# Optimization experiments

Hardware: AMD Instinct MI355X
Metric: run time of the kernel (lower is better)

## Reference

```python
import jax, jax.numpy as jnp
import numpy as np

N_NODES = 200_000
N_BONDS = 200_000
N_EDGES = 2 * N_BONDS
D_V, D_E, D_H, DEPTH = 133, 14, 200, 3


def setup_inputs() -> dict:
    key = jax.random.key(0)
    ks = jax.random.split(key, 10)
    V = jax.random.normal(ks[0], (N_NODES, D_V), dtype=jnp.float32)
    E_feat = jax.random.normal(ks[1], (N_EDGES, D_E), dtype=jnp.float32)
    # paired directed edges: edge 2b = (u,v), edge 2b+1 = (v,u)
    u = jax.random.randint(ks[2], (N_BONDS,), 0, N_NODES)
    v = jax.random.randint(ks[3], (N_BONDS,), 0, N_NODES)
    src = jnp.stack([u, v], axis=1).reshape(-1)
    dst = jnp.stack([v, u], axis=1).reshape(-1)
    edge_index = jnp.stack([src, dst], axis=0).astype(jnp.int64)
    rev_edge_index = (jnp.arange(N_EDGES) ^ 1).astype(jnp.int64)
    s = 0.05
    W_i = jax.random.normal(ks[4], (D_V + D_E, D_H), dtype=jnp.float32) * s
    b_i = jax.random.normal(ks[5], (D_H,), dtype=jnp.float32) * s
    W_h = jax.random.normal(ks[6], (D_H, D_H), dtype=jnp.float32) * s
    b_h = jax.random.normal(ks[7], (D_H,), dtype=jnp.float32) * s
    W_o = jax.random.normal(ks[8], (D_V + D_H, D_H), dtype=jnp.float32) * s
    b_o = jax.random.normal(ks[9], (D_H,), dtype=jnp.float32) * s
    return {"V": V, "E_feat": E_feat, "edge_index": edge_index,
            "rev_edge_index": rev_edge_index, "W_i": W_i, "b_i": b_i,
            "W_h": W_h, "b_h": b_h, "W_o": W_o, "b_o": b_o}


def reference(V, E_feat, edge_index, rev_edge_index, W_i, b_i, W_h, b_h, W_o, b_o):
    src = edge_index[0]
    dst = edge_index[1]
    n_edges = E_feat.shape[0]
    # h^(0) = relu(W_i([x_v || e_vw]))
    H0 = jax.nn.relu(jnp.concatenate([V[src], E_feat], axis=1) @ W_i + b_i)
    H = H0
    not_self_rev = (rev_edge_index != jnp.arange(n_edges))[:, None]  # [E,1]
    for _ in range(1, DEPTH):
        node_messages = jax.ops.segment_sum(H, dst, num_segments=N_NODES)  # [N,d_h]
        M = node_messages[src] - jnp.where(not_self_rev, H[rev_edge_index], 0.0)
        H = jax.nn.relu(H0 + M @ W_h + b_h)
    M_v = jax.ops.segment_sum(H, src, num_segments=N_NODES)  # [N,d_h]
    H_v = jax.nn.relu(jnp.concatenate([V, M_v], axis=1) @ W_o + b_o)
    return H_v
```

## Files before the change

kernel.cpp:

```cpp
#include <hip/hip_runtime.h>
#include <hip/hip_bf16.h>
#include <stdint.h>

typedef __hip_bfloat16 bf16;
typedef __attribute__((ext_vector_type(8))) short short8;
typedef __attribute__((ext_vector_type(4))) float f32x4;

#define NN 200000
#define NE 400000
#define DV 133
#define DE 14
#define DH 200
#define MT 128
#define NT 13
#define LDA 40
#define NCH 782

#define KI 160
#define KH 224
#define KO 352

#define MFMA(a, b, c) __builtin_amdgcn_mfma_f32_16x16x32_bf16((a), (b), (c), 0, 0, 0)

__device__ __forceinline__ float b2f(bf16 x) { return __bfloat162float(x); }
__device__ __forceinline__ float us2f(unsigned short u) {
  return __uint_as_float(((unsigned)u) << 16);
}
__device__ __forceinline__ unsigned short f2us(float f) {
  bf16 h = __float2bfloat16(f);
  return *reinterpret_cast<unsigned short*>(&h);
}

__global__ __launch_bounds__(256) void prepw_kernel(
    const float* __restrict__ W, int K, int ldk, bf16* __restrict__ out)
{
  int idx = blockIdx.x * 256 + threadIdx.x;
  int rowv = ldk >> 3;
  int total = 208 * rowv;
  if (idx >= total) return;
  int c = idx / rowv, r = idx - c * rowv;
  int k0 = r * 8;
  short8 w;
#pragma unroll
  for (int j = 0; j < 8; ++j) {
    int k = k0 + j;
    float v = (k < K && c < DH) ? W[(size_t)k * DH + c] : 0.f;
    w[j] = (short)f2us(v);
  }
  *(short8*)&((unsigned short*)out)[(size_t)c * ldk + k0] = w;
}

__global__ __launch_bounds__(256) void hist_kernel(
    const int* __restrict__ dst, int* __restrict__ counts)
{
  int e = blockIdx.x * 256 + threadIdx.x;
  if (e < NE) atomicAdd(&counts[dst[e]], 1);
}

__global__ __launch_bounds__(256) void chunksum_kernel(
    const int* __restrict__ counts, int* __restrict__ chunkSum)
{
  int b = blockIdx.x, tid = threadIdx.x;
  int i = b * 256 + tid;
  int v = (i < NN) ? counts[i] : 0;
#pragma unroll
  for (int d = 32; d; d >>= 1) v += __shfl_down(v, d, 64);
  __shared__ int ws[4];
  if ((tid & 63) == 0) ws[tid >> 6] = v;
  __syncthreads();
  if (tid == 0) chunkSum[b] = ws[0] + ws[1] + ws[2] + ws[3];
}

__global__ __launch_bounds__(1024) void scanchunks_kernel(
    const int* __restrict__ chunkSum, int* __restrict__ chunkOff)
{
  __shared__ int s[1024];
  int tid = threadIdx.x;
  int v = (tid < NCH) ? chunkSum[tid] : 0;
  s[tid] = v;
  __syncthreads();
  for (int d = 1; d < 1024; d <<= 1) {
    int t = (tid >= d) ? s[tid - d] : 0;
    __syncthreads();
    s[tid] += t;
    __syncthreads();
  }
  if (tid < NCH) chunkOff[tid] = s[tid] - v;
}

__global__ __launch_bounds__(256) void scanlocal_kernel(
    const int* __restrict__ counts, const int* __restrict__ chunkOff,
    int* __restrict__ offsets, int* __restrict__ cursor)
{
  __shared__ int s[256];
  int b = blockIdx.x, tid = threadIdx.x;
  int i = b * 256 + tid;
  int v = (i < NN) ? counts[i] : 0;
  s[tid] = v;
  __syncthreads();
  for (int d = 1; d < 256; d <<= 1) {
    int t = (tid >= d) ? s[tid - d] : 0;
    __syncthreads();
    s[tid] += t;
    __syncthreads();
  }
  if (i < NN) {
    int off = chunkOff[b] + s[tid] - v;
    offsets[i] = off;
    cursor[i] = off;
  }
  if (i == 0) offsets[NN] = NE;
}

__global__ __launch_bounds__(256) void scatter_kernel(
    const int* __restrict__ dst, int* __restrict__ cursor, int* __restrict__ perm)
{
  int e = blockIdx.x * 256 + threadIdx.x;
  if (e < NE) {
    int p = atomicAdd(&cursor[dst[e]], 1);
    perm[p] = e;
  }
}

__global__ __launch_bounds__(256) void h0_kernel(
    const float* __restrict__ V, const float* __restrict__ Ef,
    const int* __restrict__ src,
    const bf16* __restrict__ WiT,
    const float* __restrict__ bi,
    bf16* __restrict__ H0)
{
  __shared__ __align__(16) unsigned short AsS[MT * LDA];
  __shared__ __align__(16) unsigned short WtS[208 * LDA];
  __shared__ int Ssrc[MT];
  __shared__ float Sb[DH];
  const int tid = threadIdx.x;
  const int e0 = blockIdx.x * MT;
  if (tid < MT) Ssrc[tid] = src[e0 + tid];
  if (tid < DH) Sb[tid] = bi[tid];
  const int wv = tid >> 6, ln = tid & 15, q = (tid & 63) >> 4;
  f32x4 acc[NT][2];
#pragma unroll
  for (int t = 0; t < NT; ++t)
#pragma unroll
    for (int m = 0; m < 2; ++m) acc[t][m] = (f32x4){0.f, 0.f, 0.f, 0.f};
  const int K = DV + DE;
  const unsigned short* Wp = (const unsigned short*)WiT;
  __syncthreads();
  for (int k0 = 0; k0 < KI; k0 += 32) {
    for (int idx = tid; idx < 832; idx += 256) {
      int c = idx >> 2, kg = idx & 3;
      *(short8*)&WtS[c * LDA + kg * 8] =
          *(const short8*)&Wp[(size_t)c * KI + k0 + kg * 8];
    }
    {
      int rr = tid >> 1, half = tid & 1;
      int e = e0 + rr, s = Ssrc[rr];
      int kb = k0 + half * 16;
      unsigned short av[16];
#pragma unroll
      for (int j = 0; j < 16; ++j) {
        int k = kb + j;
        float a = 0.f;
        if (k < DV) a = V[(size_t)s * DV + k];
        else if (k < K) a = Ef[(size_t)e * DE + (k - DV)];
        av[j] = f2us(a);
      }
      short8 w0, w1;
#pragma unroll
      for (int j = 0; j < 8; ++j) { w0[j] = (short)av[j]; w1[j] = (short)av[8 + j]; }
      *(short8*)&AsS[rr * LDA + half * 16] = w0;
      *(short8*)&AsS[rr * LDA + half * 16 + 8] = w1;
    }
    __syncthreads();
    {
      short8 a0 = *(const short8*)&AsS[(wv * 32 + ln) * LDA + q * 8];
      short8 a1 = *(const short8*)&AsS[(wv * 32 + 16 + ln) * LDA + q * 8];
#pragma unroll
      for (int t = 0; t < NT; ++t) {
        short8 b = *(const short8*)&WtS[(t * 16 + ln) * LDA + q * 8];
        acc[t][0] = MFMA(a0, b, acc[t][0]);
        acc[t][1] = MFMA(a1, b, acc[t][1]);
      }
    }
    __syncthreads();
  }
#pragma unroll
  for (int t = 0; t < NT; ++t) {
    int c = t * 16 + ln;
    if (c < DH) {
#pragma unroll
      for (int m = 0; m < 2; ++m)
#pragma unroll
        for (int i = 0; i < 4; ++i) {
          int e = e0 + wv * 32 + m * 16 + q * 4 + i;
          float h = acc[t][m][i] + Sb[c];
          H0[(size_t)e * DH + c] = __float2bfloat16(h > 0.f ? h : 0.f);
        }
    }
  }
}

__global__ __launch_bounds__(256) void gemmq_kernel(
    const bf16* __restrict__ H,
    const bf16* __restrict__ WhT,
    bf16* __restrict__ Q)
{
  __shared__ __align__(16) unsigned short AsS[MT * LDA];
  __shared__ __align__(16) unsigned short WtS[208 * LDA];
  const int tid = threadIdx.x;
  const int e0 = blockIdx.x * MT;
  const int wv = tid >> 6, ln = tid & 15, q = (tid & 63) >> 4;
  f32x4 acc[NT][2];
#pragma unroll
  for (int t = 0; t < NT; ++t)
#pragma unroll
    for (int m = 0; m < 2; ++m) acc[t][m] = (f32x4){0.f, 0.f, 0.f, 0.f};
  const unsigned short* Hs = (const unsigned short*)H;
  const unsigned short* Wp = (const unsigned short*)WhT;
  for (int k0 = 0; k0 < KH; k0 += 32) {
    for (int idx = tid; idx < 832; idx += 256) {
      int c = idx >> 2, kg = idx & 3;
      *(short8*)&WtS[c * LDA + kg * 8] =
          *(const short8*)&Wp[(size_t)c * KH + k0 + kg * 8];
    }
    for (int idx = tid; idx < 512; idx += 256) {
      int rr = idx >> 2, kg = idx & 3;
      *(short8*)&AsS[rr * LDA + kg * 8] =
          *(const short8*)&Hs[(size_t)(e0 + rr) * DH + k0 + kg * 8];
    }
    __syncthreads();
    {
      short8 a0 = *(const short8*)&AsS[(wv * 32 + ln) * LDA + q * 8];
      short8 a1 = *(const short8*)&AsS[(wv * 32 + 16 + ln) * LDA + q * 8];
#pragma unroll
      for (int t = 0; t < NT; ++t) {
        short8 b = *(const short8*)&WtS[(t * 16 + ln) * LDA + q * 8];
        acc[t][0] = MFMA(a0, b, acc[t][0]);
        acc[t][1] = MFMA(a1, b, acc[t][1]);
      }
    }
    __syncthreads();
  }
#pragma unroll
  for (int t = 0; t < NT; ++t) {
    int c = t * 16 + ln;
    if (c < DH) {
#pragma unroll
      for (int m = 0; m < 2; ++m)
#pragma unroll
        for (int i = 0; i < 4; ++i) {
          int e = e0 + wv * 32 + m * 16 + q * 4 + i;
          Q[(size_t)e * DH + c] = __float2bfloat16(acc[t][m][i]);
        }
    }
  }
}

__global__ __launch_bounds__(256) void fusedmp_kernel(
    const bf16* __restrict__ Q, const bf16* H0,
    const int* __restrict__ offsets, const int* __restrict__ perm,
    const float* __restrict__ bh, bf16* Hout)
{
  int t = blockIdx.x * 256 + threadIdx.x;
  if (t >= NN * 25) return;
  int n = t / 25, g = t - n * 25;
  int st = offsets[n], en = offsets[n + 1];
  if (st == en) return;
  const unsigned short* Qs = (const unsigned short*)Q;
  const unsigned short* H0s = (const unsigned short*)H0;
  unsigned short* Os = (unsigned short*)Hout;
  float a[8];
  const float4* bp = (const float4*)(bh + g * 8);
  float4 b0 = bp[0], b1 = bp[1];
  a[0] = b0.x; a[1] = b0.y; a[2] = b0.z; a[3] = b0.w;
  a[4] = b1.x; a[5] = b1.y; a[6] = b1.z; a[7] = b1.w;
  for (int j = st; j < en; ++j) {
    int e = perm[j];
    short8 u = *(const short8*)(Qs + (size_t)e * DH + g * 8);
#pragma unroll
    for (int k = 0; k < 8; ++k) a[k] += us2f((unsigned short)u[k]);
  }
  for (int j = st; j < en; ++j) {
    int e = perm[j];
    int eo = e ^ 1;
    short8 uq = *(const short8*)(Qs + (size_t)e * DH + g * 8);
    short8 uh = *(const short8*)(H0s + (size_t)eo * DH + g * 8);
    short8 w;
#pragma unroll
    for (int k = 0; k < 8; ++k) {
      float h = a[k] - us2f((unsigned short)uq[k]) + us2f((unsigned short)uh[k]);
      w[k] = (short)f2us(h > 0.f ? h : 0.f);
    }
    *(short8*)(Os + (size_t)eo * DH + g * 8) = w;
  }
}

__global__ __launch_bounds__(256) void gather_kernel(
    const bf16* __restrict__ H, const int* __restrict__ offsets,
    const int* __restrict__ perm, int xm, float* __restrict__ nm)
{
  int t = blockIdx.x * 256 + threadIdx.x;
  if (t >= NN * 25) return;
  int n = t / 25, g = t - n * 25;
  int st = offsets[n], en = offsets[n + 1];
  float a[8];
#pragma unroll
  for (int k = 0; k < 8; ++k) a[k] = 0.f;
  const unsigned short* Hs = (const unsigned short*)H;
  for (int j = st; j < en; ++j) {
    int e = perm[j] ^ xm;
    short8 u = *(const short8*)(Hs + (size_t)e * DH + g * 8);
#pragma unroll
    for (int k = 0; k < 8; ++k) a[k] += us2f((unsigned short)u[k]);
  }
  float4* o = (float4*)(nm + (size_t)n * DH + g * 8);
  o[0] = make_float4(a[0], a[1], a[2], a[3]);
  o[1] = make_float4(a[4], a[5], a[6], a[7]);
}

__global__ __launch_bounds__(256) void out_kernel(
    const float* __restrict__ V, const float* __restrict__ Mv,
    const bf16* __restrict__ WoT,
    const float* __restrict__ bo,
    float* __restrict__ out)
{
  __shared__ __align__(16) unsigned short AsS[MT * LDA];
  __shared__ __align__(16) unsigned short WtS[208 * LDA];
  __shared__ float Sb[DH];
  const int tid = threadIdx.x;
  const int n0 = blockIdx.x * MT;
  if (tid < DH) Sb[tid] = bo[tid];
  const int wv = tid >> 6, ln = tid & 15, q = (tid & 63) >> 4;
  f32x4 acc[NT][2];
#pragma unroll
  for (int t = 0; t < NT; ++t)
#pragma unroll
    for (int m = 0; m < 2; ++m) acc[t][m] = (f32x4){0.f, 0.f, 0.f, 0.f};
  const int K = DV + DH;
  const unsigned short* Wp = (const unsigned short*)WoT;
  __syncthreads();
  for (int k0 = 0; k0 < KO; k0 += 32) {
    for (int idx = tid; idx < 832; idx += 256) {
      int c = idx >> 2, kg = idx & 3;
      *(short8*)&WtS[c * LDA + kg * 8] =
          *(const short8*)&Wp[(size_t)c * KO + k0 + kg * 8];
    }
    {
      int rr = tid >> 1, half = tid & 1;
      int n = n0 + rr;
      int kb = k0 + half * 16;
      unsigned short av[16];
      if (n < NN) {
#pragma unroll
        for (int j = 0; j < 16; ++j) {
          int k = kb + j;
          float a = 0.f;
          if (k < DV) a = V[(size_t)n * DV + k];
          else if (k < K) a = Mv[(size_t)n * DH + (k - DV)];
          av[j] = f2us(a);
        }
      } else {
#pragma unroll
        for (int j = 0; j < 16; ++j) av[j] = 0;
      }
      short8 w0, w1;
#pragma unroll
      for (int j = 0; j < 8; ++j) { w0[j] = (short)av[j]; w1[j] = (short)av[8 + j]; }
      *(short8*)&AsS[rr * LDA + half * 16] = w0;
      *(short8*)&AsS[rr * LDA + half * 16 + 8] = w1;
    }
    __syncthreads();
    {
      short8 a0 = *(const short8*)&AsS[(wv * 32 + ln) * LDA + q * 8];
      short8 a1 = *(const short8*)&AsS[(wv * 32 + 16 + ln) * LDA + q * 8];
#pragma unroll
      for (int t = 0; t < NT; ++t) {
        short8 b = *(const short8*)&WtS[(t * 16 + ln) * LDA + q * 8];
        acc[t][0] = MFMA(a0, b, acc[t][0]);
        acc[t][1] = MFMA(a1, b, acc[t][1]);
      }
    }
    __syncthreads();
  }
#pragma unroll
  for (int t = 0; t < NT; ++t) {
    int c = t * 16 + ln;
    if (c < DH) {
#pragma unroll
      for (int m = 0; m < 2; ++m)
#pragma unroll
        for (int i = 0; i < 4; ++i) {
          int n = n0 + wv * 32 + m * 16 + q * 4 + i;
          if (n < NN) {
            float h = acc[t][m][i] + Sb[c];
            out[(size_t)n * DH + c] = h > 0.f ? h : 0.f;
          }
        }
    }
  }
}

extern "C" void kernel_launch(void* const* d_in, const int* in_sizes, int n_in,
                              void* d_out, int out_size, void* d_ws, size_t ws_size,
                              hipStream_t stream)
{
  const float* V  = (const float*)d_in[0];
  const float* Ef = (const float*)d_in[1];
  const int* eidx = (const int*)d_in[2];
  const int* rev  = (const int*)d_in[3];   (void)rev;
  const float* Wi = (const float*)d_in[4];
  const float* bi = (const float*)d_in[5];
  const float* Wh = (const float*)d_in[6];
  const float* bh = (const float*)d_in[7];
  const float* Wo = (const float*)d_in[8];
  const float* bo = (const float*)d_in[9];
  const int* src = eidx;
  const int* dst = eidx + NE;

  bf16* H0 = (bf16*)d_ws;
  bf16* Hb = H0 + (size_t)NE * DH;
  bf16* Q  = Hb + (size_t)NE * DH;
  float* nm = (float*)Q;
  int* counts   = (int*)(Q + (size_t)NE * DH);
  int* chunkSum = counts + NN;
  int* chunkOff = chunkSum + 1024;
  int* offsets  = chunkOff + 1024;
  int* cursor   = offsets + NN + 1;
  int* perm     = cursor + NN;
  bf16* WiT = (bf16*)(((uintptr_t)(perm + NE) + 15) & ~(uintptr_t)15);
  bf16* WhT = WiT + 208 * KI;
  bf16* WoT = WhT + 208 * KH;

  const int gGE = NE / MT;
  const int gON = (NN + MT - 1) / MT;
  const int gE  = (NE + 255) / 256;
  const int gN  = (NN + 255) / 256;
  const int gG  = (NN * 25 + 255) / 256;

  hipMemsetAsync(counts, 0, (size_t)NN * sizeof(int), stream);
  hist_kernel<<<gE, 256, 0, stream>>>(dst, counts);
  chunksum_kernel<<<NCH, 256, 0, stream>>>(counts, chunkSum);
  scanchunks_kernel<<<1, 1024, 0, stream>>>(chunkSum, chunkOff);
  scanlocal_kernel<<<gN, 256, 0, stream>>>(counts, chunkOff, offsets, cursor);
  scatter_kernel<<<gE, 256, 0, stream>>>(dst, cursor, perm);

  prepw_kernel<<<(208 * KI / 8 + 255) / 256, 256, 0, stream>>>(Wi, DV + DE, KI, WiT);
  prepw_kernel<<<(208 * KH / 8 + 255) / 256, 256, 0, stream>>>(Wh, DH, KH, WhT);
  prepw_kernel<<<(208 * KO / 8 + 255) / 256, 256, 0, stream>>>(Wo, DV + DH, KO, WoT);

  h0_kernel<<<gGE, 256, 0, stream>>>(V, Ef, src, WiT, bi, H0);

  gemmq_kernel<<<gGE, 256, 0, stream>>>(H0, WhT, Q);
  fusedmp_kernel<<<gG, 256, 0, stream>>>(Q, H0, offsets, perm, bh, Hb);

  gemmq_kernel<<<gGE, 256, 0, stream>>>(Hb, WhT, Q);
  fusedmp_kernel<<<gG, 256, 0, stream>>>(Q, H0, offsets, perm, bh, H0);

  gather_kernel<<<gG, 256, 0, stream>>>(H0, offsets, perm, 1, nm);
  out_kernel<<<gON, 256, 0, stream>>>(V, nm, WoT, bo, (float*)d_out);
}
```

Measured before the change: 1.392 ms.

## Pre-pack V and output GEMM operand as padded bf16 rows for vectorized loads

Adds a pass that converts V to a bf16 buffer padded to 160 columns. The h0 GEMM gathers source-node rows from it with 16-byte vector loads instead of scalar fp32 loads and per-element conversion. For the output stage, the gather kernel writes M_v as bf16 straight into a combined [M_v || V] padded operand, with Wo rows reordered to match, so out_kernel streams A tiles with vector loads. This costs extra pack kernels, and the workspace buffers are reused, which adds aliasing risk.

```diff
diff --git a/kernel.cpp b/kernel.cpp
--- a/kernel.cpp
+++ b/kernel.cpp
@@ -7,6 +7,7 @@
 typedef __attribute__((ext_vector_type(4))) float f32x4;
 
 #define NN 200000
+#define NNPAD 200064
 #define NE 400000
 #define DV 133
 #define DE 14
@@ -19,10 +20,10 @@
 #define KI 160
 #define KH 224
 #define KO 352
+#define LDV 160
 
 #define MFMA(a, b, c) __builtin_amdgcn_mfma_f32_16x16x32_bf16((a), (b), (c), 0, 0, 0)
 
-__device__ __forceinline__ float b2f(bf16 x) { return __bfloat162float(x); }
 __device__ __forceinline__ float us2f(unsigned short u) {
   return __uint_as_float(((unsigned)u) << 16);
 }
@@ -48,6 +49,60 @@
     w[j] = (short)f2us(v);
   }
   *(short8*)&((unsigned short*)out)[(size_t)c * ldk + k0] = w;
+}
+
+__global__ __launch_bounds__(256) void prepwo_kernel(
+    const float* __restrict__ Wo, bf16* __restrict__ out)
+{
+  int idx = blockIdx.x * 256 + threadIdx.x;
+  int total = 208 * (KO >> 3);
+  if (idx >= total) return;
+  int c = idx / (KO >> 3), r = idx - c * (KO >> 3);
+  int k0 = r * 8;
+  short8 w;
+#pragma unroll
+  for (int j = 0; j < 8; ++j) {
+    int k = k0 + j;
+    int sr = (k < 200) ? (133 + k) : (k - 200);
+    float v = (k < 333 && c < DH) ? Wo[(size_t)sr * DH + c] : 0.f;
+    w[j] = (short)f2us(v);
+  }
+  *(short8*)&((unsigned short*)out)[(size_t)c * KO + k0] = w;
+}
+
+__global__ __launch_bounds__(256) void packv_kernel(
+    const float* __restrict__ V, unsigned short* __restrict__ Vb)
+{
+  int idx = blockIdx.x * 256 + threadIdx.x;
+  if (idx >= NN * (LDV / 8)) return;
+  int n = idx / (LDV / 8), g = idx - n * (LDV / 8);
+  int k0 = g * 8;
+  short8 w;
+#pragma unroll
+  for (int j = 0; j < 8; ++j) {
+    int k = k0 + j;
+    float v = (k < DV) ? V[(size_t)n * DV + k] : 0.f;
+    w[j] = (short)f2us(v);
+  }
+  *(short8*)&Vb[(size_t)n * LDV + k0] = w;
+}
+
+__global__ __launch_bounds__(256) void packav_kernel(
+    const float* __restrict__ V, unsigned short* __restrict__ Abuf)
+{
+  int idx = blockIdx.x * 256 + threadIdx.x;
+  if (idx >= NNPAD * (KO / 8)) return;
+  int n = idx / (KO / 8), g = idx - n * (KO / 8);
+  int k0 = g * 8;
+  if (n < NN && k0 < 200) return;
+  short8 w;
+#pragma unroll
+  for (int j = 0; j < 8; ++j) {
+    int k = k0 + j;
+    float v = (n < NN && k >= 200 && k < 333) ? V[(size_t)n * DV + (k - 200)] : 0.f;
+    w[j] = (short)f2us(v);
+  }
+  *(short8*)&Abuf[(size_t)n * KO + k0] = w;
 }
 
 __global__ __launch_bounds__(256) void hist_kernel(
@@ -123,7 +178,8 @@
 }
 
 __global__ __launch_bounds__(256) void h0_kernel(
-    const float* __restrict__ V, const float* __restrict__ Ef,
+    const unsigned short* __restrict__ Vb,
+    const float* __restrict__ Ef,
     const int* __restrict__ src,
     const bf16* __restrict__ WiT,
     const float* __restrict__ bi,
@@ -143,10 +199,35 @@
   for (int t = 0; t < NT; ++t)
 #pragma unroll
     for (int m = 0; m < 2; ++m) acc[t][m] = (f32x4){0.f, 0.f, 0.f, 0.f};
-  const int K = DV + DE;
   const unsigned short* Wp = (const unsigned short*)WiT;
   __syncthreads();
-  for (int k0 = 0; k0 < KI; k0 += 32) {
+  for (int k0 = 0; k0 < 128; k0 += 32) {
+    for (int idx = tid; idx < 832; idx += 256) {
+      int c = idx >> 2, kg = idx & 3;
+      *(short8*)&WtS[c * LDA + kg * 8] =
+          *(const short8*)&Wp[(size_t)c * KI + k0 + kg * 8];
+    }
+    for (int idx = tid; idx < 512; idx += 256) {
+      int rr = idx >> 2, kg = idx & 3;
+      int s = Ssrc[rr];
+      *(short8*)&AsS[rr * LDA + kg * 8] =
+          *(const short8*)&Vb[(size_t)s * LDV + k0 + kg * 8];
+    }
+    __syncthreads();
+    {
+      short8 a0 = *(const short8*)&AsS[(wv * 32 + ln) * LDA + q * 8];
+      short8 a1 = *(const short8*)&AsS[(wv * 32 + 16 + ln) * LDA + q * 8];
+#pragma unroll
+      for (int t = 0; t < NT; ++t) {
+        short8 b = *(const short8*)&WtS[(t * 16 + ln) * LDA + q * 8];
+        acc[t][0] = MFMA(a0, b, acc[t][0]);
+        acc[t][1] = MFMA(a1, b, acc[t][1]);
+      }
+    }
+    __syncthreads();
+  }
+  {
+    const int k0 = 128;
     for (int idx = tid; idx < 832; idx += 256) {
       int c = idx >> 2, kg = idx & 3;
       *(short8*)&WtS[c * LDA + kg * 8] =
@@ -160,10 +241,10 @@
 #pragma unroll
       for (int j = 0; j < 16; ++j) {
         int k = kb + j;
-        float a = 0.f;
-        if (k < DV) a = V[(size_t)s * DV + k];
-        else if (k < K) a = Ef[(size_t)e * DE + (k - DV)];
-        av[j] = f2us(a);
+        unsigned short x = 0;
+        if (k < DV) x = Vb[(size_t)s * LDV + k];
+        else if (k < DV + DE) x = f2us(Ef[(size_t)e * DE + (k - DV)]);
+        av[j] = x;
       }
       short8 w0, w1;
 #pragma unroll
@@ -297,7 +378,7 @@
 
 __global__ __launch_bounds__(256) void gather_kernel(
     const bf16* __restrict__ H, const int* __restrict__ offsets,
-    const int* __restrict__ perm, int xm, float* __restrict__ nm)
+    const int* __restrict__ perm, int xm, unsigned short* __restrict__ Abuf)
 {
   int t = blockIdx.x * 256 + threadIdx.x;
   if (t >= NN * 25) return;
@@ -313,13 +394,14 @@
 #pragma unroll
     for (int k = 0; k < 8; ++k) a[k] += us2f((unsigned short)u[k]);
   }
-  float4* o = (float4*)(nm + (size_t)n * DH + g * 8);
-  o[0] = make_float4(a[0], a[1], a[2], a[3]);
-  o[1] = make_float4(a[4], a[5], a[6], a[7]);
+  short8 w;
+#pragma unroll
+  for (int k = 0; k < 8; ++k) w[k] = (short)f2us(a[k]);
+  *(short8*)&Abuf[(size_t)n * KO + g * 8] = w;
 }
 
 __global__ __launch_bounds__(256) void out_kernel(
-    const float* __restrict__ V, const float* __restrict__ Mv,
+    const unsigned short* __restrict__ Abuf,
     const bf16* __restrict__ WoT,
     const float* __restrict__ bo,
     float* __restrict__ out)
@@ -336,7 +418,6 @@
   for (int t = 0; t < NT; ++t)
 #pragma unroll
     for (int m = 0; m < 2; ++m) acc[t][m] = (f32x4){0.f, 0.f, 0.f, 0.f};
-  const int K = DV + DH;
   const unsigned short* Wp = (const unsigned short*)WoT;
   __syncthreads();
   for (int k0 = 0; k0 < KO; k0 += 32) {
@@ -345,29 +426,10 @@
       *(short8*)&WtS[c * LDA + kg * 8] =
           *(const short8*)&Wp[(size_t)c * KO + k0 + kg * 8];
     }
-    {
-      int rr = tid >> 1, half = tid & 1;
-      int n = n0 + rr;
-      int kb = k0 + half * 16;
-      unsigned short av[16];
-      if (n < NN) {
-#pragma unroll
-        for (int j = 0; j < 16; ++j) {
-          int k = kb + j;
-          float a = 0.f;
-          if (k < DV) a = V[(size_t)n * DV + k];
-          else if (k < K) a = Mv[(size_t)n * DH + (k - DV)];
-          av[j] = f2us(a);
-        }
-      } else {
-#pragma unroll
-        for (int j = 0; j < 16; ++j) av[j] = 0;
-      }
-      short8 w0, w1;
-#pragma unroll
-      for (int j = 0; j < 8; ++j) { w0[j] = (short)av[j]; w1[j] = (short)av[8 + j]; }
-      *(short8*)&AsS[rr * LDA + half * 16] = w0;
-      *(short8*)&AsS[rr * LDA + half * 16 + 8] = w1;
+    for (int idx = tid; idx < 512; idx += 256) {
+      int rr = idx >> 2, kg = idx & 3;
+      *(short8*)&AsS[rr * LDA + kg * 8] =
+          *(const short8*)&Abuf[(size_t)(n0 + rr) * KO + k0 + kg * 8];
     }
     __syncthreads();
     {
@@ -420,7 +482,8 @@
   bf16* H0 = (bf16*)d_ws;
   bf16* Hb = H0 + (size_t)NE * DH;
   bf16* Q  = Hb + (size_t)NE * DH;
-  float* nm = (float*)Q;
+  unsigned short* Vb16 = (unsigned short*)Hb;
+  unsigned short* Abuf = (unsigned short*)Q;
   int* counts   = (int*)(Q + (size_t)NE * DH);
   int* chunkSum = counts + NN;
   int* chunkOff = chunkSum + 1024;
@@ -446,9 +509,11 @@
 
   prepw_kernel<<<(208 * KI / 8 + 255) / 256, 256, 0, stream>>>(Wi, DV + DE, KI, WiT);
   prepw_kernel<<<(208 * KH / 8 + 255) / 256, 256, 0, stream>>>(Wh, DH, KH, WhT);
-  prepw_kernel<<<(208 * KO / 8 + 255) / 256, 256, 0, stream>>>(Wo, DV + DH, KO, WoT);
-
-  h0_kernel<<<gGE, 256, 0, stream>>>(V, Ef, src, WiT, bi, H0);
+  prepwo_kernel<<<(208 * KO / 8 + 255) / 256, 256, 0, stream>>>(Wo, WoT);
+
+  packv_kernel<<<(NN * (LDV / 8) + 255) / 256, 256, 0, stream>>>(V, Vb16);
+
+  h0_kernel<<<gGE, 256, 0, stream>>>(Vb16, Ef, src, WiT, bi, H0);
 
   gemmq_kernel<<<gGE, 256, 0, stream>>>(H0, WhT, Q);
   fusedmp_kernel<<<gG, 256, 0, stream>>>(Q, H0, offsets, perm, bh, Hb);
@@ -456,6 +521,8 @@
   gemmq_kernel<<<gGE, 256, 0, stream>>>(Hb, WhT, Q);
   fusedmp_kernel<<<gG, 256, 0, stream>>>(Q, H0, offsets, perm, bh, H0);
 
-  gather_kernel<<<gG, 256, 0, stream>>>(H0, offsets, perm, 1, nm);
-  out_kernel<<<gON, 256, 0, stream>>>(V, nm, WoT, bo, (float*)d_out);
-}
+  packav_kernel<<<(NNPAD * (KO / 8) + 255) / 256, 256, 0, stream>>>(V, Abuf);
+
+  gather_kernel<<<gG, 256, 0, stream>>>(H0, offsets, perm, 1, Abuf);
+  out_kernel<<<gON, 256, 0, stream>>>(Abuf, WoT, bo, (float*)d_out);
+}
```

Measured after the change: 1.370 ms. No clear change (-1.6%).
